# Kernel tuning notes

Hardware: AMD Instinct MI355X
Metric: run time of the kernel (lower is better)

## Reference

```python
import jax, jax.numpy as jnp
import numpy as np

N_NODES = 100000
N_EDGES = 1200000
D_IN = 64
D_HID = 64


def _gcn_layer(h_in, W, b, src, dst, norm, n_nodes):
    # h_in: [N, d_in]; W: [d_in, d_out]; norm: [E_total] symmetric deg norm
    h = h_in @ W                                  # [N, d_out]
    msg = h[src] * norm[:, None]                  # gather + scale, [E_total, d_out]
    agg = jax.ops.segment_sum(msg, dst, num_segments=n_nodes)  # scatter-add
    return agg + b


def _prelu(x, a):
    # per-channel PReLU: a broadcasts over nodes
    return jnp.where(x >= 0, x, a * x)


def setup_inputs() -> dict:
    key = jax.random.key(0)
    ks = jax.random.split(key, 8)
    x = jax.random.normal(ks[0], (N_NODES, D_IN), dtype=jnp.float32)
    edge_index = jax.random.randint(ks[1], (2, N_EDGES), 0, N_NODES, dtype=jnp.int64)
    # Glorot-ish weights, PyG GCNConv defaults: weight + bias; PReLU init slope 0.25
    W1 = jax.random.normal(ks[2], (D_IN, D_HID), dtype=jnp.float32) / np.sqrt(D_IN)
    b1 = jnp.zeros((D_HID,), dtype=jnp.float32)
    a1 = jnp.full((D_HID,), 0.25, dtype=jnp.float32)
    W2 = jax.random.normal(ks[3], (D_HID, D_HID), dtype=jnp.float32) / np.sqrt(D_HID)
    b2 = jnp.zeros((D_HID,), dtype=jnp.float32)
    a2 = jnp.full((D_HID,), 0.25, dtype=jnp.float32)
    return {"x": x, "edge_index": edge_index, "W1": W1, "b1": b1, "a1": a1,
            "W2": W2, "b2": b2, "a2": a2}


def reference(x, edge_index, W1, b1, a1, W2, b2, a2):
    n = x.shape[0]
    # add self-loops (GCNConv default add_self_loops=True)
    loops = jnp.arange(n, dtype=edge_index.dtype)
    src = jnp.concatenate([edge_index[0], loops])
    dst = jnp.concatenate([edge_index[1], loops])
    # symmetric normalization: deg computed on destination with unit edge weights
    deg = jax.ops.segment_sum(jnp.ones_like(src, dtype=x.dtype), dst, num_segments=n)
    dinv = jnp.where(deg > 0, jax.lax.rsqrt(deg), 0.0)
    norm = dinv[src] * dinv[dst]                  # [E + N]

    h = _gcn_layer(x, W1, b1, src, dst, norm, n)
    h = _prelu(h, a1)
    h = _gcn_layer(h, W2, b2, src, dst, norm, n)
    h = _prelu(h, a2)
    return h
```

## Files before the change

### kernel.cpp

```cpp
#include <hip/hip_runtime.h>
#include <hip/hip_bf16.h>
#include <hip/hip_fp16.h>

#define D 64
#define GXN 16
#define NB 256
#define BSHIFT 8
#define SUBS 4
#define SCAP 1024
#define CHUNK 4096
#define AGN 32
#define BFSTRIDE 16


__global__ void __launch_bounds__(256, 4)
k_bin_gemm(const int* __restrict__ src, const int* __restrict__ dst,
           unsigned* __restrict__ records, int* __restrict__ bucket_fill,
           int E, int nbin,
           const float* __restrict__ X, const float* __restrict__ W,
           __half* __restrict__ H, int n, int ntiles, int gemmb) {
    __shared__ int cnt[512];
    __shared__ int gbase[512];
    const int t = threadIdx.x;

    if ((int)blockIdx.x < nbin) {
        const int slot = blockIdx.x & (SUBS - 1);
        cnt[t] = 0; cnt[t + 256] = 0;
        __syncthreads();

        const int base_e = blockIdx.x * CHUNK;
        unsigned rec[16];
        unsigned br[16];
#pragma unroll
        for (int i = 0; i < 16; ++i) {
            int e = base_e + i * 256 + t;
            if (e < E) {
                int s = src[e], d = dst[e];
                int bk = d >> BSHIFT;
                rec[i] = ((unsigned)s << BSHIFT) | (unsigned)(d & (NB - 1));
                int rank = atomicAdd(&cnt[bk], 1);
                br[i] = ((unsigned)bk << 16) | (unsigned)rank;
            } else {
                br[i] = 0xFFFFFFFFu;
            }
        }
        __syncthreads();
#pragma unroll
        for (int rep = 0; rep < 2; ++rep) {
            int bk = t + rep * 256;
            if (cnt[bk] > 0)
                gbase[bk] = atomicAdd(&bucket_fill[(bk * SUBS + slot) * BFSTRIDE], cnt[bk]);
        }
        __syncthreads();
#pragma unroll
        for (int i = 0; i < 16; ++i) {
            if (br[i] != 0xFFFFFFFFu) {
                int bk = br[i] >> 16;
                int idx = gbase[bk] + (int)(br[i] & 0xFFFF);
                if (idx < SCAP)
                    records[((size_t)bk * SUBS + slot) * SCAP + idx] = rec[i];
            }
        }
    } else {
        const int lane = t & 63;
        const int wv   = t >> 6;
        float wreg[64];
#pragma unroll
        for (int k = 0; k < D; ++k) wreg[k] = W[k * D + lane];

        const int bid = blockIdx.x - nbin;
        for (int tile = bid; tile < ntiles; tile += gemmb) {
            const int nb4 = tile * GXN + wv * 4;
            const int ln  = nb4 + (lane >> 4);
            float4 xv = make_float4(0.f, 0.f, 0.f, 0.f);
            if (ln < n)
                xv = *reinterpret_cast<const float4*>(X + (size_t)ln * D + (lane & 15) * 4);
            float xc[4] = {xv.x, xv.y, xv.z, xv.w};
#pragma unroll
            for (int g = 0; g < 4; ++g) {
                const int node = nb4 + g;
                if (node >= n) break;
                float acc = 0.f;
#pragma unroll
                for (int k = 0; k < D; ++k) {
                    float xk = __uint_as_float(__builtin_amdgcn_readlane(
                        __float_as_uint(xc[k & 3]), g * 16 + (k >> 2)));
                    acc = fmaf(xk, wreg[k], acc);
                }
                H[(size_t)node * D + lane] = __float2half_rn(acc);
            }
        }
    }
}


__global__ void k_csr(const unsigned* __restrict__ records,
                      const int* __restrict__ bucket_fill,
                      int* __restrict__ rowptr, float* __restrict__ dinv,
                      int* __restrict__ csr_src, __half* __restrict__ H,
                      int n, int E) {
    __shared__ int bscan[256];
    __shared__ int binc[512];
    __shared__ int cnt[NB];
    __shared__ int excl[NB];
    __shared__ float ddi[NB];
    __shared__ int stage[SUBS * SCAP];

    const int t = threadIdx.x;
    const int b = blockIdx.x;
    const int nbuckets = gridDim.x;

    int s0 = 0, s1 = 0;
#pragma unroll
    for (int s = 0; s < SUBS; ++s) {
        if (2 * t     < nbuckets) s0 += bucket_fill[((2 * t)     * SUBS + s) * BFSTRIDE];
        if (2 * t + 1 < nbuckets) s1 += bucket_fill[((2 * t + 1) * SUBS + s) * BFSTRIDE];
    }
    bscan[t] = s0 + s1;
    __syncthreads();
    for (int off = 1; off < 256; off <<= 1) {
        int val = bscan[t];
        if (t >= off) val += bscan[t - off];
        __syncthreads();
        bscan[t] = val;
        __syncthreads();
    }
    {
        int ep = bscan[t] - (s0 + s1);
        binc[2 * t]     = ep + s0;
        binc[2 * t + 1] = ep + s0 + s1;
    }
    __syncthreads();
    const int base  = (b == 0) ? 0 : binc[b - 1];
    if (b == nbuckets - 1 && t == 0) rowptr[n] = binc[nbuckets - 1];

    int subcnt[SUBS];
    int cnt_e = 0;
#pragma unroll
    for (int s = 0; s < SUBS; ++s) {
        subcnt[s] = bucket_fill[(b * SUBS + s) * BFSTRIDE];
        cnt_e += subcnt[s];
    }

    cnt[t] = 0;
    __syncthreads();
#pragma unroll
    for (int s = 0; s < SUBS; ++s) {
        const size_t so = ((size_t)b * SUBS + s) * SCAP;
        for (int i = t; i < subcnt[s]; i += 256)
            atomicAdd(&cnt[records[so + i] & (NB - 1)], 1);
    }
    __syncthreads();

    const int c0 = cnt[t];
    bscan[t] = c0;
    __syncthreads();
    for (int off = 1; off < 256; off <<= 1) {
        int val = bscan[t];
        if (t >= off) val += bscan[t - off];
        __syncthreads();
        bscan[t] = val;
        __syncthreads();
    }
    excl[t] = bscan[t] - c0;
    {
        int node = b * NB + t;
        float di = rsqrtf((float)(c0 + 1));
        ddi[t] = di;
        if (node < n) {
            rowptr[node] = base + excl[t];
            dinv[node]   = di;
        }
        cnt[t] = 0;
    }
    __syncthreads();

#pragma unroll
    for (int s = 0; s < SUBS; ++s) {
        const size_t so = ((size_t)b * SUBS + s) * SCAP;
        for (int i = t; i < subcnt[s]; i += 256) {
            unsigned r = records[so + i];
            int d8 = r & (NB - 1);
            int rank = atomicAdd(&cnt[d8], 1);
            stage[excl[d8] + rank] = (int)(r >> BSHIFT);
        }
    }
    __syncthreads();

    for (int i = t; i < cnt_e; i += 256)
        csr_src[base + i] = stage[i];

#pragma unroll
    for (int r = 0; r < (NB * 8) / 256; ++r) {
        int idx = r * 256 + t;
        int nl = idx >> 3;
        int node = b * NB + nl;
        if (node < n) {
            int part = (idx & 7) * 8;
            uint4 g = *reinterpret_cast<uint4*>(H + (size_t)node * D + part);
            __half2* p = reinterpret_cast<__half2*>(&g);
            float s = ddi[nl];
#pragma unroll
            for (int i = 0; i < 4; ++i) {
                float2 f = __half22float2(p[i]);
                p[i] = __floats2half2_rn(f.x * s, f.y * s);
            }
            *reinterpret_cast<uint4*>(H + (size_t)node * D + part) = g;
        }
    }
}

__device__ __forceinline__ void edge_accum(const __half* __restrict__ Hn,
                                           const int* __restrict__ csr_src,
                                           int beg, int end, int part, float acc[8]) {
    int idx[8];
#pragma unroll
    for (int j = 0; j < 8; ++j)
        idx[j] = (beg + j < end) ? csr_src[beg + j] : 0;
    int k = beg;
    while (k < end) {
        int s[8];
        float w[8];
#pragma unroll
        for (int j = 0; j < 8; ++j) {
            s[j] = idx[j];
            w[j] = (k + j < end) ? 1.f : 0.f;
        }
        int kn = k + 8;
#pragma unroll
        for (int j = 0; j < 8; ++j)
            idx[j] = (kn + j < end) ? csr_src[kn + j] : 0;
        uint4 g[8];
#pragma unroll
        for (int j = 0; j < 8; ++j)
            g[j] = *reinterpret_cast<const uint4*>(Hn + (size_t)s[j] * D + part);
#pragma unroll
        for (int j = 0; j < 8; ++j) {
            const __half2* p = reinterpret_cast<const __half2*>(&g[j]);
#pragma unroll
            for (int i = 0; i < 4; ++i) {
                float2 f = __half22float2(p[i]);
                acc[2 * i + 0] += w[j] * f.x;
                acc[2 * i + 1] += w[j] * f.y;
            }
        }
        k = kn;
    }
}


__global__ void k_agg_gemm(const __half* __restrict__ Hn1,
                           const int* __restrict__ rowptr,
                           const int* __restrict__ csr_src,
                           const float* __restrict__ dinv,
                           const float* __restrict__ b1, const float* __restrict__ a1,
                           const float* __restrict__ W2,
                           __half* __restrict__ Hn2, int n) {
    __shared__ float W2l[D * D];
    __shared__ float Yl[AGN][68];

    const int t = threadIdx.x;
    for (int i = t; i < (D * D) / 4; i += 256)
        *reinterpret_cast<float4*>(W2l + i * 4) = *reinterpret_cast<const float4*>(W2 + i * 4);

    const int nl   = t >> 3;
    const int part = (t & 7) * 8;
    const int node = blockIdx.x * AGN + nl;

    float di = 0.f;
    if (node < n) {
        di = dinv[node];
        float acc[8];
        {
            uint4 g = *reinterpret_cast<const uint4*>(Hn1 + (size_t)node * D + part);
            const __half2* p = reinterpret_cast<const __half2*>(&g);
#pragma unroll
            for (int i = 0; i < 4; ++i) {
                float2 f = __half22float2(p[i]);
                acc[2 * i + 0] = f.x;
                acc[2 * i + 1] = f.y;
            }
        }
        edge_accum(Hn1, csr_src, rowptr[node], rowptr[node + 1], part, acc);

        const float4 b0 = *reinterpret_cast<const float4*>(b1 + part);
        const float4 b4 = *reinterpret_cast<const float4*>(b1 + part + 4);
        const float4 a0 = *reinterpret_cast<const float4*>(a1 + part);
        const float4 a4 = *reinterpret_cast<const float4*>(a1 + part + 4);
        float y0 = acc[0] * di + b0.x, y1 = acc[1] * di + b0.y;
        float y2 = acc[2] * di + b0.z, y3 = acc[3] * di + b0.w;
        float y4 = acc[4] * di + b4.x, y5 = acc[5] * di + b4.y;
        float y6 = acc[6] * di + b4.z, y7 = acc[7] * di + b4.w;
        Yl[nl][part + 0] = (y0 >= 0.f) ? y0 : a0.x * y0;
        Yl[nl][part + 1] = (y1 >= 0.f) ? y1 : a0.y * y1;
        Yl[nl][part + 2] = (y2 >= 0.f) ? y2 : a0.z * y2;
        Yl[nl][part + 3] = (y3 >= 0.f) ? y3 : a0.w * y3;
        Yl[nl][part + 4] = (y4 >= 0.f) ? y4 : a4.x * y4;
        Yl[nl][part + 5] = (y5 >= 0.f) ? y5 : a4.y * y5;
        Yl[nl][part + 6] = (y6 >= 0.f) ? y6 : a4.z * y6;
        Yl[nl][part + 7] = (y7 >= 0.f) ? y7 : a4.w * y7;
    }
    __syncthreads();

    if (node >= n) return;
    float o[8];
#pragma unroll
    for (int i = 0; i < 8; ++i) o[i] = 0.f;
#pragma unroll 8
    for (int k = 0; k < D; ++k) {
        float yk = Yl[nl][k];
        float4 w0 = *reinterpret_cast<const float4*>(W2l + k * D + part);
        float4 w1 = *reinterpret_cast<const float4*>(W2l + k * D + part + 4);
        o[0] += yk * w0.x; o[1] += yk * w0.y; o[2] += yk * w0.z; o[3] += yk * w0.w;
        o[4] += yk * w1.x; o[5] += yk * w1.y; o[6] += yk * w1.z; o[7] += yk * w1.w;
    }
    __half2 h0 = __floats2half2_rn(o[0] * di, o[1] * di);
    __half2 h1 = __floats2half2_rn(o[2] * di, o[3] * di);
    __half2 h2 = __floats2half2_rn(o[4] * di, o[5] * di);
    __half2 h3 = __floats2half2_rn(o[6] * di, o[7] * di);
    uint4 pack;
    pack.x = *reinterpret_cast<unsigned int*>(&h0);
    pack.y = *reinterpret_cast<unsigned int*>(&h1);
    pack.z = *reinterpret_cast<unsigned int*>(&h2);
    pack.w = *reinterpret_cast<unsigned int*>(&h3);
    *reinterpret_cast<uint4*>(Hn2 + (size_t)node * D + part) = pack;
}


__global__ void k_aggregate(const __half* __restrict__ Hn,
                            const int* __restrict__ rowptr,
                            const int* __restrict__ csr_src,
                            const float* __restrict__ dinv,
                            const float* __restrict__ b, const float* __restrict__ a,
                            float* __restrict__ out, int n) {
    int t = blockIdx.x * blockDim.x + threadIdx.x;
    int node = t >> 3;
    if (node >= n) return;
    int part = (t & 7) * 8;

    float di = dinv[node];
    float acc[8];
    {
        uint4 g = *reinterpret_cast<const uint4*>(Hn + (size_t)node * D + part);
        const __half2* p = reinterpret_cast<const __half2*>(&g);
#pragma unroll
        for (int i = 0; i < 4; ++i) {
            float2 f = __half22float2(p[i]);
            acc[2 * i + 0] = f.x;
            acc[2 * i + 1] = f.y;
        }
    }
    edge_accum(Hn, csr_src, rowptr[node], rowptr[node + 1], part, acc);

    const float4 b0 = *reinterpret_cast<const float4*>(b + part);
    const float4 b4 = *reinterpret_cast<const float4*>(b + part + 4);
    const float4 a0 = *reinterpret_cast<const float4*>(a + part);
    const float4 a4 = *reinterpret_cast<const float4*>(a + part + 4);
    float4 r0, r1;
    r0.x = acc[0] * di + b0.x; r0.y = acc[1] * di + b0.y;
    r0.z = acc[2] * di + b0.z; r0.w = acc[3] * di + b0.w;
    r1.x = acc[4] * di + b4.x; r1.y = acc[5] * di + b4.y;
    r1.z = acc[6] * di + b4.z; r1.w = acc[7] * di + b4.w;
    r0.x = (r0.x >= 0.f) ? r0.x : a0.x * r0.x;
    r0.y = (r0.y >= 0.f) ? r0.y : a0.y * r0.y;
    r0.z = (r0.z >= 0.f) ? r0.z : a0.z * r0.z;
    r0.w = (r0.w >= 0.f) ? r0.w : a0.w * r0.w;
    r1.x = (r1.x >= 0.f) ? r1.x : a4.x * r1.x;
    r1.y = (r1.y >= 0.f) ? r1.y : a4.y * r1.y;
    r1.z = (r1.z >= 0.f) ? r1.z : a4.z * r1.z;
    r1.w = (r1.w >= 0.f) ? r1.w : a4.w * r1.w;
    float* o = out + (size_t)node * D + part;
    *reinterpret_cast<float4*>(o) = r0;
    *reinterpret_cast<float4*>(o + 4) = r1;
}

extern "C" void kernel_launch(void* const* d_in, const int* in_sizes, int n_in,
                              void* d_out, int out_size, void* d_ws, size_t ws_size,
                              hipStream_t stream) {
    const float* x  = (const float*)d_in[0];
    const int*   ei = (const int*)  d_in[1];
    const float* W1 = (const float*)d_in[2];
    const float* b1 = (const float*)d_in[3];
    const float* a1 = (const float*)d_in[4];
    const float* W2 = (const float*)d_in[5];
    const float* b2 = (const float*)d_in[6];
    const float* a2 = (const float*)d_in[7];
    float* out = (float*)d_out;

    const int n   = in_sizes[0] / D;
    const int E   = in_sizes[1] / 2;
    const int n64 = n * D;

    const int* src = ei;
    const int* dst = ei + E;

    const int nbuckets = (n + NB - 1) >> BSHIFT;

    int*      bucket_fill = (int*)d_ws;
    unsigned* records     = (unsigned*)(bucket_fill + 2048 * BFSTRIDE);
    int*      rowptr      = (int*)(records + (size_t)nbuckets * SUBS * SCAP);
    float*    dinv        = (float*)(rowptr + ((n + 257) & ~255));
    int*      csr_src     = (int*)(dinv + ((n + 256) & ~255));
    __half*   Hn1         = (__half*)(csr_src + ((E + 255) & ~255));
    __half*   Hn2         = Hn1 + (((size_t)n64 + 256) & ~(size_t)255);

    const int B = 256;
    const int nbin   = (E + CHUNK - 1) / CHUNK;
    const int gemmb  = 1024;
    const int ntiles = (n + GXN - 1) / GXN;

    hipMemsetAsync(bucket_fill, 0, 2048 * BFSTRIDE * sizeof(int), stream);

    k_bin_gemm<<<nbin + gemmb, B, 0, stream>>>(src, dst, records, bucket_fill, E, nbin,
                                               x, W1, Hn1, n, ntiles, gemmb);
    k_csr<<<nbuckets, B, 0, stream>>>(records, bucket_fill, rowptr, dinv, csr_src,
                                      Hn1, n, E);
    k_agg_gemm<<<(n + AGN - 1) / AGN, B, 0, stream>>>(Hn1, rowptr, csr_src, dinv,
                                                      b1, a1, W2, Hn2, n);
    k_aggregate<<<(n * 8 + B - 1) / B, B, 0, stream>>>(Hn2, rowptr, csr_src, dinv,
                                                       b2, a2, out, n);
}
```

Measured before the change: 201.2 us.

## Use split-fp16 MFMA for first-layer GEMM and double binning sub-slots

Replaces the scalar FMA plus readlane GEMM in the fused binning/GEMM kernel with 16x16x32 fp16 MFMA instructions. Each wave now computes a 16-node tile, and the work-stealing grid is halved. To keep close to fp32 accuracy, X and W are split into high and low fp16 parts, costing three MFMAs per k-step. Separately, the number of per-bucket sub-slots for edge binning goes from 4 to 8, which spreads the atomic counters and adds record capacity per bucket, at the cost of a larger workspace and a larger memset.

```diff
diff --git a/kernel.cpp b/kernel.cpp
--- a/kernel.cpp
+++ b/kernel.cpp
@@ -3,14 +3,16 @@
 #include <hip/hip_fp16.h>
 
 #define D 64
-#define GXN 16
 #define NB 256
 #define BSHIFT 8
-#define SUBS 4
+#define SUBS 8
 #define SCAP 1024
 #define CHUNK 4096
 #define AGN 32
 #define BFSTRIDE 16
+
+typedef _Float16 f16x8 __attribute__((ext_vector_type(8)));
+typedef float    f32x4 __attribute__((ext_vector_type(4)));
 
 
 __global__ void __launch_bounds__(256, 4)
@@ -64,31 +66,66 @@
     } else {
         const int lane = t & 63;
         const int wv   = t >> 6;
-        float wreg[64];
-#pragma unroll
-        for (int k = 0; k < D; ++k) wreg[k] = W[k * D + lane];
-
-        const int bid = blockIdx.x - nbin;
-        for (int tile = bid; tile < ntiles; tile += gemmb) {
-            const int nb4 = tile * GXN + wv * 4;
-            const int ln  = nb4 + (lane >> 4);
-            float4 xv = make_float4(0.f, 0.f, 0.f, 0.f);
-            if (ln < n)
-                xv = *reinterpret_cast<const float4*>(X + (size_t)ln * D + (lane & 15) * 4);
-            float xc[4] = {xv.x, xv.y, xv.z, xv.w};
-#pragma unroll
-            for (int g = 0; g < 4; ++g) {
-                const int node = nb4 + g;
-                if (node >= n) break;
-                float acc = 0.f;
-#pragma unroll
-                for (int k = 0; k < D; ++k) {
-                    float xk = __uint_as_float(__builtin_amdgcn_readlane(
-                        __float_as_uint(xc[k & 3]), g * 16 + (k >> 2)));
-                    acc = fmaf(xk, wreg[k], acc);
+        const int r16  = lane & 15;
+        const int g4   = lane >> 4;
+
+        f16x8 Bh[4][2], Bl[4][2];
+#pragma unroll
+        for (int ct = 0; ct < 4; ++ct)
+#pragma unroll
+            for (int kt = 0; kt < 2; ++kt)
+#pragma unroll
+                for (int j = 0; j < 8; ++j) {
+                    float w = W[(kt * 32 + g4 * 8 + j) * D + ct * 16 + r16];
+                    _Float16 h = (_Float16)w;
+                    Bh[ct][kt][j] = h;
+                    Bl[ct][kt][j] = (_Float16)(w - (float)h);
                 }
-                H[(size_t)node * D + lane] = __float2half_rn(acc);
-            }
+
+        const int gw = (blockIdx.x - nbin) * 4 + wv;
+        for (int tile = gw; tile < ntiles; tile += gemmb * 4) {
+            const int nb16 = tile * 16;
+            int row = nb16 + r16;
+            if (row > n - 1) row = n - 1;
+            const float* xp = X + (size_t)row * D + g4 * 8;
+            float4 x0 = *reinterpret_cast<const float4*>(xp);
+            float4 x1 = *reinterpret_cast<const float4*>(xp + 4);
+            float4 x2 = *reinterpret_cast<const float4*>(xp + 32);
+            float4 x3 = *reinterpret_cast<const float4*>(xp + 36);
+            float xs[16] = {x0.x, x0.y, x0.z, x0.w, x1.x, x1.y, x1.z, x1.w,
+                            x2.x, x2.y, x2.z, x2.w, x3.x, x3.y, x3.z, x3.w};
+            f16x8 Ah[2], Al[2];
+#pragma unroll
+            for (int kt = 0; kt < 2; ++kt)
+#pragma unroll
+                for (int j = 0; j < 8; ++j) {
+                    float v = xs[kt * 8 + j];
+                    _Float16 h = (_Float16)v;
+                    Ah[kt][j] = h;
+                    Al[kt][j] = (_Float16)(v - (float)h);
+                }
+
+            f32x4 acc[4];
+#pragma unroll
+            for (int ct = 0; ct < 4; ++ct)
+                acc[ct] = (f32x4){0.f, 0.f, 0.f, 0.f};
+#pragma unroll
+            for (int ct = 0; ct < 4; ++ct) {
+#pragma unroll
+                for (int kt = 0; kt < 2; ++kt) {
+                    acc[ct] = __builtin_amdgcn_mfma_f32_16x16x32_f16(Ah[kt], Bh[ct][kt], acc[ct], 0, 0, 0);
+                    acc[ct] = __builtin_amdgcn_mfma_f32_16x16x32_f16(Al[kt], Bh[ct][kt], acc[ct], 0, 0, 0);
+                    acc[ct] = __builtin_amdgcn_mfma_f32_16x16x32_f16(Ah[kt], Bl[ct][kt], acc[ct], 0, 0, 0);
+                }
+            }
+#pragma unroll
+            for (int ct = 0; ct < 4; ++ct)
+#pragma unroll
+                for (int r = 0; r < 4; ++r) {
+                    int node = nb16 + g4 * 4 + r;
+                    if (node < n)
+                        H[(size_t)node * D + ct * 16 + r16] = __float2half_rn(acc[ct][r]);
+                }
         }
     }
 }
@@ -397,7 +434,7 @@
     const int nbuckets = (n + NB - 1) >> BSHIFT;
 
     int*      bucket_fill = (int*)d_ws;
-    unsigned* records     = (unsigned*)(bucket_fill + 2048 * BFSTRIDE);
+    unsigned* records     = (unsigned*)(bucket_fill + 4096 * BFSTRIDE);
     int*      rowptr      = (int*)(records + (size_t)nbuckets * SUBS * SCAP);
     float*    dinv        = (float*)(rowptr + ((n + 257) & ~255));
     int*      csr_src     = (int*)(dinv + ((n + 256) & ~255));
@@ -406,10 +443,10 @@
 
     const int B = 256;
     const int nbin   = (E + CHUNK - 1) / CHUNK;
-    const int gemmb  = 1024;
-    const int ntiles = (n + GXN - 1) / GXN;
-
-    hipMemsetAsync(bucket_fill, 0, 2048 * BFSTRIDE * sizeof(int), stream);
+    const int gemmb  = 512;
+    const int ntiles = (n + 15) / 16;
+
+    hipMemsetAsync(bucket_fill, 0, 4096 * BFSTRIDE * sizeof(int), stream);
 
     k_bin_gemm<<<nbin + gemmb, B, 0, stream>>>(src, dst, records, bucket_fill, E, nbin,
                                                x, W1, Hn1, n, ntiles, gemmb);
```

New measurement: 184.5 us. -8.3%, faster.
